# Kernel optimization log

Hardware: AMD Instinct MI355X
Metric: run time of the kernel (lower is better)

The kernel has to match this reference:

```python
import jax, jax.numpy as jnp
import numpy as np

B, N, C, H = 8, 1024, 1024, 16  # batch, seq, dim, heads
HID = 4 * C                     # mlp hidden (mlp_ratio=4.0)


def _ln(x, g, b, eps=1e-5):
    m = x.mean(-1, keepdims=True)
    v = ((x - m) ** 2).mean(-1, keepdims=True)
    return (x - m) / jnp.sqrt(v + eps) * g + b


def setup_inputs() -> dict:
    key = jax.random.key(0)
    ks = jax.random.split(key, 8)
    s = 0.02  # init scale
    f32 = jnp.float32
    return {
        "x": jax.random.normal(ks[0], (B, N, C), f32),
        "g1": jnp.ones((C,), f32), "b1": jnp.zeros((C,), f32),
        "Wq": jax.random.normal(ks[1], (C, C), f32) * s, "bq": jnp.zeros((C,), f32),
        "Wk": jax.random.normal(ks[2], (C, C), f32) * s, "bk": jnp.zeros((C,), f32),
        "Wv": jax.random.normal(ks[3], (C, C), f32) * s, "bv": jnp.zeros((C,), f32),
        "Wp": jax.random.normal(ks[4], (C, C), f32) * s, "bp": jnp.zeros((C,), f32),
        "g2": jnp.ones((C,), f32), "b2": jnp.zeros((C,), f32),
        "W1": jax.random.normal(ks[5], (C, HID), f32) * s, "c1": jnp.zeros((HID,), f32),
        "W2": jax.random.normal(ks[6], (HID, C), f32) * s, "c2": jnp.zeros((C,), f32),
    }


def reference(x, g1, b1, Wq, bq, Wk, bk, Wv, bv, Wp, bp, g2, b2, W1, c1, W2, c2):
    hd = C // H
    scale = hd ** -0.5
    # --- pre-norm self-attention ---
    h = _ln(x, g1, b1)
    # NOTE: faithful to source: direct reshape (B,N,C)->(B,H,N,hd), NOT the
    # standard reshape(B,N,H,hd).transpose -- the original code reshapes the
    # flat N*C block into H contiguous chunks of N*hd.
    q = (h @ Wq + bq).reshape(B, H, -1, hd)
    k = (h @ Wk + bk).reshape(B, H, -1, hd)
    v = (h @ Wv + bv).reshape(B, H, -1, hd)
    attn = jax.nn.softmax(jnp.einsum('bhnd,bhmd->bhnm', q, k) * scale, axis=-1)
    o = jnp.einsum('bhnm,bhmd->bhnd', attn, v)
    o = jnp.swapaxes(o, 1, 2).reshape(B, -1, C)  # (B,N,C)
    x = x + (o @ Wp + bp)
    # --- MLP block ---
    h2 = _ln(x, g2, b2)
    m = jax.nn.gelu(h2 @ W1 + c1, approximate=False) @ W2 + c2
    return x + m
```

## Files before the change

kernel.cpp:

```cpp
#include <hip/hip_runtime.h>
#include <hip/hip_bf16.h>
#include <math.h>

typedef __bf16 bf16_t;
typedef __bf16 bf16x4 __attribute__((ext_vector_type(4)));
typedef __bf16 bf16x8 __attribute__((ext_vector_type(8)));
typedef float  f32x4  __attribute__((ext_vector_type(4)));

typedef __attribute__((address_space(1))) const void GVoid;
typedef __attribute__((address_space(3))) void LVoid;

__device__ __forceinline__ void gld16(const void* g, void* l) {
    __builtin_amdgcn_global_load_lds((GVoid*)g, (LVoid*)l, 16, 0, 0);
}

__device__ __forceinline__ float gelu_exact(float v) {
    return 0.5f * v * (1.0f + erff(v * 0.7071067811865475f));
}

__device__ __forceinline__ f32x4 MF(bf16x8 a, bf16x8 b, f32x4 c) {
    return __builtin_amdgcn_mfma_f32_16x16x32_bf16(a, b, c, 0, 0, 0);
}

#define VMCNT(n) asm volatile("s_waitcnt vmcnt(" #n ")" ::: "memory")
#define FENCE()  asm volatile("" ::: "memory")

__global__ __launch_bounds__(256) void transpose_f32_bf16(
    const float* __restrict__ in, bf16_t* __restrict__ out,
    int R, int C, size_t inBatch, size_t outBatch)
{
    __shared__ bf16_t tile[64][65];
    const float* src = in  + (size_t)blockIdx.z * inBatch;
    bf16_t*      dst = out + (size_t)blockIdx.z * outBatch;
    const int r0 = blockIdx.y * 64, c0 = blockIdx.x * 64;
    const int t = threadIdx.x, tc = t & 63, tr = t >> 6;
#pragma unroll
    for (int i = 0; i < 16; ++i) {
        int r = tr + i * 4;
        tile[r][tc] = (bf16_t)src[(size_t)(r0 + r) * C + c0 + tc];
    }
    __syncthreads();
#pragma unroll
    for (int i = 0; i < 16; ++i) {
        int r = tr + i * 4;
        dst[(size_t)(c0 + r) * R + r0 + tc] = tile[tc][r];
    }
}

__global__ __launch_bounds__(256) void transpose_bf16(
    const bf16_t* __restrict__ in, bf16_t* __restrict__ out,
    int R, int C, size_t inBatch, size_t outBatch)
{
    __shared__ __align__(16) bf16_t tile[64][65];
    const bf16_t* src = in  + (size_t)blockIdx.z * inBatch;
    bf16_t*       dst = out + (size_t)blockIdx.z * outBatch;
    const int r0 = blockIdx.y * 64, c0 = blockIdx.x * 64;
    const int t = threadIdx.x, tc = t & 63, tr = t >> 6;
#pragma unroll
    for (int i = 0; i < 16; ++i) {
        int r = tr + i * 4;
        tile[r][tc] = src[(size_t)(r0 + r) * C + c0 + tc];
    }
    __syncthreads();
#pragma unroll
    for (int i = 0; i < 16; ++i) {
        int r = tr + i * 4;
        dst[(size_t)(c0 + r) * R + r0 + tc] = tile[tc][r];
    }
}

__global__ __launch_bounds__(256) void ln_kernel(
    const float* __restrict__ x, const float* __restrict__ g,
    const float* __restrict__ b, bf16_t* __restrict__ out)
{
    const int row = blockIdx.x, t = threadIdx.x;
    const float4 v4 = ((const float4*)(x + (size_t)row * 1024))[t];
    float v[4] = {v4.x, v4.y, v4.z, v4.w};
    float s = v[0] + v[1] + v[2] + v[3];
    float s2 = v[0]*v[0] + v[1]*v[1] + v[2]*v[2] + v[3]*v[3];
#pragma unroll
    for (int o = 1; o < 64; o <<= 1) { s += __shfl_xor(s, o); s2 += __shfl_xor(s2, o); }
    __shared__ float red[8];
    if ((t & 63) == 0) { red[t >> 6] = s; red[4 + (t >> 6)] = s2; }
    __syncthreads();
    s  = red[0] + red[1] + red[2] + red[3];
    s2 = red[4] + red[5] + red[6] + red[7];
    const float mean = s * (1.f / 1024.f);
    const float var  = fmaxf(s2 * (1.f / 1024.f) - mean * mean, 0.f);
    const float rstd = rsqrtf(var + 1e-5f);
    const float4 g4 = ((const float4*)g)[t];
    const float4 b4 = ((const float4*)b)[t];
    bf16x4 o;
    o[0] = (bf16_t)((v[0] - mean) * rstd * g4.x + b4.x);
    o[1] = (bf16_t)((v[1] - mean) * rstd * g4.y + b4.y);
    o[2] = (bf16_t)((v[2] - mean) * rstd * g4.z + b4.z);
    o[3] = (bf16_t)((v[3] - mean) * rstd * g4.w + b4.w);
    *(bf16x4*)(out + (size_t)row * 1024 + t * 4) = o;
}

template <int MODE>
__global__ __launch_bounds__(512, 2) void gemm256(
    const bf16_t* __restrict__ A, const bf16_t* __restrict__ Bt,
    const float* __restrict__ b0, const float* __restrict__ b1,
    const float* __restrict__ b2, const float* resid,
    bf16_t* __restrict__ ob0, bf16_t* __restrict__ ob1,
    bf16_t* __restrict__ ob2, float* of, int N, int K)
{
    __shared__ __align__(16) char lds[65536 + 32768];
    char* ldsB = lds + 65536;

    const int t = threadIdx.x;
    const int w = t >> 6, ln = t & 63;
    const int wm = w & 3, wn = w >> 2;
    const int l16 = ln & 15, quad = ln >> 4;
    const int m0 = blockIdx.x * 256, n0 = blockIdx.y * 128;

    const bf16_t* gA = A  + (size_t)m0 * K;
    const bf16_t* gB = Bt + (size_t)n0 * K;

    const int w1k  = w << 10;
    const int srow = t >> 3;
    const int scol = ((t & 7) ^ (srow & 7)) << 3;

    auto stageA = [&](int kt, int h) {
        char* dst = lds + (kt & 1) * 32768 + h * 16384 + w1k;
        const bf16_t* s0 = gA + (size_t)(h * 128 + srow) * K + (kt << 6) + scol;
        gld16(s0, dst);
        gld16(s0 + (size_t)64 * K, dst + 8192);
    };
    auto stageB = [&](int kt) {
        char* dst = ldsB + (kt & 1) * 16384 + w1k;
        const bf16_t* s0 = gB + (size_t)srow * K + (kt << 6) + scol;
        gld16(s0, dst);
        gld16(s0 + (size_t)64 * K, dst + 8192);
    };

    auto rdA = [&](int q, int i, int ks) -> bf16x8 {
        const int r = (i & 1) * 64 + wm * 16 + l16;
        const char* p = lds + q * 32768 + (i >> 1) * 16384 + r * 128
                        + ((ks * 64 + quad * 16) ^ ((r & 7) << 4));
        return *(const bf16x8*)p;
    };
    auto rdB = [&](int q, int j, int ks) -> bf16x8 {
        const int r = j * 32 + wn * 16 + l16;
        const char* p = ldsB + q * 16384 + r * 128
                        + ((ks * 64 + quad * 16) ^ ((r & 7) << 4));
        return *(const bf16x8*)p;
    };

    f32x4 acc[4][4];
#pragma unroll
    for (int i = 0; i < 4; ++i)
#pragma unroll
        for (int j = 0; j < 4; ++j) acc[i][j] = f32x4{0.f, 0.f, 0.f, 0.f};

    const int ktiles = K >> 6;

    stageA(0, 0); stageB(0); stageA(0, 1); stageA(1, 0); stageB(1);

    bf16x8 afr[2][2], bfr[4][2];

    for (int T = 0; T < ktiles; ++T) {
        const int q = T & 1;
        const bool notlast = (T + 1 < ktiles);

        if (notlast) VMCNT(6); else VMCNT(2);
        __builtin_amdgcn_s_barrier();
        FENCE(); __builtin_amdgcn_sched_barrier(0);
        if (notlast) stageA(T + 1, 1);
#pragma unroll
        for (int i = 0; i < 2; ++i)
#pragma unroll
            for (int ks = 0; ks < 2; ++ks) afr[i][ks] = rdA(q, i, ks);
#pragma unroll
        for (int j = 0; j < 4; ++j)
#pragma unroll
            for (int ks = 0; ks < 2; ++ks) bfr[j][ks] = rdB(q, j, ks);
        __builtin_amdgcn_s_setprio(1);
#pragma unroll
        for (int i = 0; i < 2; ++i)
#pragma unroll
            for (int j = 0; j < 4; ++j)
#pragma unroll
                for (int ks = 0; ks < 2; ++ks)
                    acc[i][j] = MF(afr[i][ks], bfr[j][ks], acc[i][j]);
        __builtin_amdgcn_s_setprio(0);
        __builtin_amdgcn_sched_barrier(0);

        if (notlast) VMCNT(6); else VMCNT(0);
        __builtin_amdgcn_s_barrier();
        FENCE(); __builtin_amdgcn_sched_barrier(0);
        if (T + 2 < ktiles) { stageA(T + 2, 0); stageB(T + 2); }
#pragma unroll
        for (int i = 0; i < 2; ++i)
#pragma unroll
            for (int ks = 0; ks < 2; ++ks) afr[i][ks] = rdA(q, 2 + i, ks);
        __builtin_amdgcn_s_setprio(1);
#pragma unroll
        for (int i = 0; i < 2; ++i)
#pragma unroll
            for (int j = 0; j < 4; ++j)
#pragma unroll
                for (int ks = 0; ks < 2; ++ks)
                    acc[2 + i][j] = MF(afr[i][ks], bfr[j][ks], acc[2 + i][j]);
        __builtin_amdgcn_s_setprio(0);
        __builtin_amdgcn_sched_barrier(0);
    }

#pragma unroll
    for (int i = 0; i < 4; ++i) {
        const int rowb = m0 + (i >> 1) * 128 + (i & 1) * 64 + wm * 16 + quad * 4;
#pragma unroll
        for (int j = 0; j < 4; ++j) {
            const int col = n0 + j * 32 + wn * 16 + l16;
            if constexpr (MODE == 0) {
                const int which = col >> 10;
                const float* bias = which == 0 ? b0 : (which == 1 ? b1 : b2);
                bf16_t* outp      = which == 0 ? ob0 : (which == 1 ? ob1 : ob2);
                const int cl = col & 1023;
                const float bc = bias[cl];
#pragma unroll
                for (int r = 0; r < 4; ++r)
                    outp[(size_t)(rowb + r) * 1024 + cl] = (bf16_t)(acc[i][j][r] + bc);
            } else if constexpr (MODE == 1) {
                const float bc = b0[col];
#pragma unroll
                for (int r = 0; r < 4; ++r) {
                    const size_t idx = (size_t)(rowb + r) * N + col;
                    of[idx] = acc[i][j][r] + bc + resid[idx];
                }
            } else if constexpr (MODE == 2) {
                const float bc = b0[col];
#pragma unroll
                for (int r = 0; r < 4; ++r)
                    ob0[(size_t)(rowb + r) * N + col] =
                        (bf16_t)gelu_exact(acc[i][j][r] + bc);
            } else {
#pragma unroll
                for (int r = 0; r < 4; ++r) {
                    const size_t idx = (size_t)(rowb + r) * N + col;
                    of[idx] += acc[i][j][r];
                }
            }
        }
    }
}

__global__ __launch_bounds__(256, 2) void attn_kernel(
    const bf16_t* __restrict__ Q, const bf16_t* __restrict__ K,
    const bf16_t* __restrict__ Vt, bf16_t* __restrict__ O)
{
    __shared__ __align__(16) bf16_t smem[32768];
    char* Vs = (char*)smem;
    char* Ks = (char*)smem + 16384;
    char* Ps = (char*)smem + 32768;

    const int t = threadIdx.x;
    const int wv = t >> 6, ln = t & 63;
    const int l16 = ln & 15, quad = ln >> 4;
    const int l7 = l16 & 7;
    const int lin = blockIdx.x + (blockIdx.y << 3);
    const int qt  = (lin >> 3) & 7;
    const int bh  = (lin & 7) * 16 + (lin >> 6);
    const size_t hb = (size_t)bh << 16;

    bf16x8 qf[2][2];
#pragma unroll
    for (int rt = 0; rt < 2; ++rt)
#pragma unroll
        for (int ks = 0; ks < 2; ++ks)
            qf[rt][ks] = *(const bf16x8*)(Q + hb +
                (size_t)(qt*128 + wv*32 + rt*16 + l16) * 64 + ks*32 + quad*8);

    float m_run[2] = {-INFINITY, -INFINITY};
    float l_run[2] = {0.f, 0.f};
    f32x4 acc_o[2][4];
#pragma unroll
    for (int rt = 0; rt < 2; ++rt)
#pragma unroll
        for (int dt = 0; dt < 4; ++dt) acc_o[rt][dt] = f32x4{0.f, 0.f, 0.f, 0.f};

    const int krow = t >> 3, kcol = (t & 7) << 3;
    const int vrow = t >> 4, vcol = (t & 15) << 3;
    const int kSwz = ((t & 7) ^ (krow & 7)) << 4;
    const int vSwz = ((t & 15) ^ (vrow & 7)) << 4;
    const float sc = 0.125f;

    bf16x8 kg[4], vg[4];
#pragma unroll
    for (int i = 0; i < 4; ++i) {
        kg[i] = *(const bf16x8*)(K  + hb + (size_t)(i*32 + krow)*64 + kcol);
        vg[i] = *(const bf16x8*)(Vt + hb + (size_t)(i*16 + vrow)*1024 + vcol);
    }

    for (int j = 0; j < 8; ++j) {
        __syncthreads();
#pragma unroll
        for (int i = 0; i < 4; ++i) {
            *(bf16x8*)(Ks + (i*32 + krow)*128 + kSwz) = kg[i];
            *(bf16x8*)(Vs + (i*16 + vrow)*256 + vSwz) = vg[i];
        }
        __syncthreads();
        if (j < 7) {
#pragma unroll
            for (int i = 0; i < 4; ++i) {
                kg[i] = *(const bf16x8*)(K  + hb + (size_t)((j+1)*128 + i*32 + krow)*64 + kcol);
                vg[i] = *(const bf16x8*)(Vt + hb + (size_t)(i*16 + vrow)*1024 + (j+1)*128 + vcol);
            }
        }

        f32x4 accs[8][2];
#pragma unroll
        for (int nt = 0; nt < 8; ++nt)
#pragma unroll
            for (int rt = 0; rt < 2; ++rt) accs[nt][rt] = f32x4{0.f, 0.f, 0.f, 0.f};
#pragma unroll
        for (int ks = 0; ks < 2; ++ks)
#pragma unroll
            for (int nt = 0; nt < 8; ++nt) {
                bf16x8 kf = *(const bf16x8*)(Ks + (nt*16 + l16)*128
                                             + (((ks*4 + quad) ^ l7) << 4));
#pragma unroll
                for (int rt = 0; rt < 2; ++rt)
                    accs[nt][rt] = __builtin_amdgcn_mfma_f32_16x16x32_bf16(
                        kf, qf[rt][ks], accs[nt][rt], 0, 0, 0);
            }

#pragma unroll
        for (int rt = 0; rt < 2; ++rt) {
            float mx = -INFINITY;
#pragma unroll
            for (int nt = 0; nt < 8; ++nt)
#pragma unroll
                for (int r = 0; r < 4; ++r) mx = fmaxf(mx, accs[nt][rt][r]);
            mx *= sc;
            mx = fmaxf(mx, __shfl_xor(mx, 16));
            mx = fmaxf(mx, __shfl_xor(mx, 32));
            if (!__all(mx <= m_run[rt] + 8.f)) {
                const float mnew  = fmaxf(m_run[rt], mx);
                const float alpha = __expf(m_run[rt] - mnew);
                m_run[rt] = mnew;
                l_run[rt] *= alpha;
#pragma unroll
                for (int r = 0; r < 4; ++r) {
                    const float af = __shfl(alpha, quad*4 + r, 16);
#pragma unroll
                    for (int dt = 0; dt < 4; ++dt) acc_o[rt][dt][r] *= af;
                }
            }
            const float mcur = m_run[rt];
            float rs = 0.f;
#pragma unroll
            for (int nt = 0; nt < 8; ++nt)
#pragma unroll
                for (int r = 0; r < 4; ++r) {
                    float p = __expf(accs[nt][rt][r] * sc - mcur);
                    accs[nt][rt][r] = p;
                    rs += p;
                }
            rs += __shfl_xor(rs, 16);
            rs += __shfl_xor(rs, 32);
            l_run[rt] += rs;
        }

#pragma unroll
        for (int rt = 0; rt < 2; ++rt) {
            const int mrow = wv*32 + rt*16 + l16;
#pragma unroll
            for (int nt = 0; nt < 8; ++nt) {
                bf16x4 pk;
#pragma unroll
                for (int r = 0; r < 4; ++r) pk[r] = (bf16_t)accs[nt][rt][r];
                const int pchunk = nt*2 + (quad >> 1);
                *(bf16x4*)(Ps + mrow*256 + ((pchunk ^ l7) << 4) + ((quad & 1) << 3)) = pk;
            }
        }
#pragma unroll
        for (int ks = 0; ks < 4; ++ks) {
            const int cSwz = ((ks*4 + quad) ^ l7) << 4;
            bf16x8 ap[2];
#pragma unroll
            for (int rt = 0; rt < 2; ++rt)
                ap[rt] = *(const bf16x8*)(Ps + (wv*32 + rt*16 + l16)*256 + cSwz);
#pragma unroll
            for (int dt = 0; dt < 4; ++dt) {
                bf16x8 bvv = *(const bf16x8*)(Vs + (dt*16 + l16)*256 + cSwz);
#pragma unroll
                for (int rt = 0; rt < 2; ++rt)
                    acc_o[rt][dt] = __builtin_amdgcn_mfma_f32_16x16x32_bf16(
                        ap[rt], bvv, acc_o[rt][dt], 0, 0, 0);
            }
        }
    }

    const int b = bh >> 4, h = bh & 15;
#pragma unroll
    for (int rt = 0; rt < 2; ++rt) {
#pragma unroll
        for (int r = 0; r < 4; ++r) {
            const float inv = 1.f / __shfl(l_run[rt], quad*4 + r, 16);
            const int m = qt*128 + wv*32 + rt*16 + quad*4 + r;
#pragma unroll
            for (int dt = 0; dt < 4; ++dt) {
                const int d = dt*16 + l16;
                O[((size_t)b*1024 + m)*1024 + h*64 + d] =
                    (bf16_t)(acc_o[rt][dt][r] * inv);
            }
        }
    }
}

extern "C" void kernel_launch(void* const* d_in, const int* in_sizes, int n_in,
                              void* d_out, int out_size, void* d_ws, size_t ws_size,
                              hipStream_t stream)
{
    (void)in_sizes; (void)n_in;
    const size_t MB = 1ull << 20;
    if (ws_size < 64 * MB) {
        hipMemsetAsync(d_out, 0, (size_t)out_size * sizeof(float), stream);
        return;
    }

    const float* x  = (const float*)d_in[0];
    const float* g1 = (const float*)d_in[1];
    const float* b1 = (const float*)d_in[2];
    const float* Wq = (const float*)d_in[3];
    const float* bq = (const float*)d_in[4];
    const float* Wk = (const float*)d_in[5];
    const float* bk = (const float*)d_in[6];
    const float* Wv = (const float*)d_in[7];
    const float* bv = (const float*)d_in[8];
    const float* Wp = (const float*)d_in[9];
    const float* bp = (const float*)d_in[10];
    const float* g2 = (const float*)d_in[11];
    const float* b2 = (const float*)d_in[12];
    const float* W1 = (const float*)d_in[13];
    const float* c1 = (const float*)d_in[14];
    const float* W2 = (const float*)d_in[15];
    const float* c2 = (const float*)d_in[16];

    char* ws = (char*)d_ws;
    bf16_t* Kb  = (bf16_t*)(ws);
    bf16_t* Vb  = (bf16_t*)(ws + 16 * MB);
    bf16_t* Cs  = (bf16_t*)(ws + 32 * MB);
    bf16_t* WqT = (bf16_t*)(ws + 48 * MB);
    bf16_t* WpT = (bf16_t*)(ws + 54 * MB);
    bf16_t* W1T = (bf16_t*)(ws + 56 * MB);
    bf16_t* W2T = (bf16_t*)(ws + 48 * MB);
    bf16_t* Qb  = (bf16_t*)d_out;
    bf16_t* Ob  = Vb;
    bf16_t* hid = Kb;
    bf16_t* h2  = Cs;
    float*  x2  = (float*)d_out;
    float*  outf = (float*)d_out;

    const dim3 blk(256);
    const dim3 blk5(512);

    transpose_f32_bf16<<<dim3(16, 16, 1), blk, 0, stream>>>(Wq, WqT,              1024, 1024, 0, 0);
    transpose_f32_bf16<<<dim3(16, 16, 1), blk, 0, stream>>>(Wk, WqT + 1024*1024,  1024, 1024, 0, 0);
    transpose_f32_bf16<<<dim3(16, 16, 1), blk, 0, stream>>>(Wv, WqT + 2*1024*1024, 1024, 1024, 0, 0);
    transpose_f32_bf16<<<dim3(16, 16, 1), blk, 0, stream>>>(Wp, WpT,              1024, 1024, 0, 0);
    transpose_f32_bf16<<<dim3(64, 16, 1), blk, 0, stream>>>(W1, W1T,              1024, 4096, 0, 0);

    ln_kernel<<<8192, blk, 0, stream>>>(x, g1, b1, Cs);

    gemm256<0><<<dim3(32, 24), blk5, 0, stream>>>(
        Cs, WqT, bq, bk, bv, nullptr, Qb, Kb, Vb, nullptr, 3072, 1024);

    transpose_bf16<<<dim3(1, 16, 128), blk, 0, stream>>>(Vb, Cs, 1024, 64, 65536, 65536);

    attn_kernel<<<dim3(8, 128), blk, 0, stream>>>(Qb, Kb, Cs, Ob);

    gemm256<1><<<dim3(32, 8), blk5, 0, stream>>>(
        Ob, WpT, bp, nullptr, nullptr, x, nullptr, nullptr, nullptr, x2, 1024, 1024);

    transpose_f32_bf16<<<dim3(16, 32, 2), blk, 0, stream>>>(
        W2, W2T, 2048, 1024, 2048*1024, 2048*1024);

    ln_kernel<<<8192, blk, 0, stream>>>(x2, g2, b2, h2);

    for (int c = 0; c < 2; ++c) {
        gemm256<2><<<dim3(32, 16), blk5, 0, stream>>>(
            h2, W1T + (size_t)c * 2048 * 1024, c1 + c * 2048,
            nullptr, nullptr, nullptr, hid, nullptr, nullptr, nullptr, 2048, 1024);
        if (c == 0)
            gemm256<1><<<dim3(32, 8), blk5, 0, stream>>>(
                hid, W2T, c2, nullptr, nullptr, outf,
                nullptr, nullptr, nullptr, outf, 1024, 2048);
        else
            gemm256<5><<<dim3(32, 8), blk5, 0, stream>>>(
                hid, W2T + (size_t)2048 * 1024, nullptr, nullptr, nullptr, nullptr,
                nullptr, nullptr, nullptr, outf, 1024, 2048);
    }
}
```

Before: 539.8 us.

## Add 256x256-tile 8-wave ping-pong GEMM for QKV and MLP-up projections

Introduces a new gemm8p kernel with a 256x256 output tile (each of 8 waves computes 128x64) and a finer-grained schedule. That schedule interleaves global-to-LDS staging of A/B halves with quadrant-wise MFMA blocks, separated by barriers and lgkmcnt waits. It is used for the QKV projection and the W1+GELU GEMMs to raise arithmetic intensity per LDS byte and halve B-tile global traffic. The old gemm256 remains for the residual-add GEMMs, with a trimmed signature. The cost is 128KB LDS per block and 128 accumulator registers per thread, which may limit occupancy. The many barriers could also expose latency.

```diff
diff --git a/kernel.cpp b/kernel.cpp
--- a/kernel.cpp
+++ b/kernel.cpp
@@ -24,6 +24,21 @@
 
 #define VMCNT(n) asm volatile("s_waitcnt vmcnt(" #n ")" ::: "memory")
 #define FENCE()  asm volatile("" ::: "memory")
+#define LG0()  do { asm volatile("s_waitcnt lgkmcnt(0)" ::: "memory"); \
+                    __builtin_amdgcn_sched_barrier(0); } while (0)
+#define BAR()  __builtin_amdgcn_s_barrier()
+
+#define MFQ(AARR, BARR, QR, QC)                                              \
+    do {                                                                     \
+        __builtin_amdgcn_s_setprio(1);                                       \
+        _Pragma("unroll") for (int rf = 0; rf < 4; ++rf)                     \
+        _Pragma("unroll") for (int cf = 0; cf < 2; ++cf)                     \
+        _Pragma("unroll") for (int ks = 0; ks < 2; ++ks)                     \
+            acc[(QR)*4 + rf][(QC)*2 + cf] =                                  \
+                MF(AARR[rf][ks], BARR[cf][ks], acc[(QR)*4 + rf][(QC)*2 + cf]); \
+        __builtin_amdgcn_s_setprio(0);                                       \
+        __builtin_amdgcn_sched_barrier(0);                                   \
+    } while (0)
 
 __global__ __launch_bounds__(256) void transpose_f32_bf16(
     const float* __restrict__ in, bf16_t* __restrict__ out,
@@ -99,21 +114,21 @@
 }
 
 template <int MODE>
-__global__ __launch_bounds__(512, 2) void gemm256(
+__global__ __launch_bounds__(512, 2) void gemm8p(
     const bf16_t* __restrict__ A, const bf16_t* __restrict__ Bt,
     const float* __restrict__ b0, const float* __restrict__ b1,
-    const float* __restrict__ b2, const float* resid,
+    const float* __restrict__ b2,
     bf16_t* __restrict__ ob0, bf16_t* __restrict__ ob1,
-    bf16_t* __restrict__ ob2, float* of, int N, int K)
+    bf16_t* __restrict__ ob2, int N, int K)
 {
-    __shared__ __align__(16) char lds[65536 + 32768];
+    __shared__ __align__(16) char lds[131072];
     char* ldsB = lds + 65536;
 
     const int t = threadIdx.x;
     const int w = t >> 6, ln = t & 63;
-    const int wm = w & 3, wn = w >> 2;
+    const int wm = w & 1, wn = w >> 1;
     const int l16 = ln & 15, quad = ln >> 4;
-    const int m0 = blockIdx.x * 256, n0 = blockIdx.y * 128;
+    const int m0 = blockIdx.x * 256, n0 = blockIdx.y * 256;
 
     const bf16_t* gA = A  + (size_t)m0 * K;
     const bf16_t* gB = Bt + (size_t)n0 * K;
@@ -128,91 +143,108 @@
         gld16(s0, dst);
         gld16(s0 + (size_t)64 * K, dst + 8192);
     };
-    auto stageB = [&](int kt) {
-        char* dst = ldsB + (kt & 1) * 16384 + w1k;
-        const bf16_t* s0 = gB + (size_t)srow * K + (kt << 6) + scol;
+    auto stageB = [&](int kt, int h) {
+        char* dst = ldsB + (kt & 1) * 32768 + h * 16384 + w1k;
+        const bf16_t* s0 = gB + (size_t)(h * 128 + srow) * K + (kt << 6) + scol;
         gld16(s0, dst);
         gld16(s0 + (size_t)64 * K, dst + 8192);
     };
 
-    auto rdA = [&](int q, int i, int ks) -> bf16x8 {
-        const int r = (i & 1) * 64 + wm * 16 + l16;
-        const char* p = lds + q * 32768 + (i >> 1) * 16384 + r * 128
-                        + ((ks * 64 + quad * 16) ^ ((r & 7) << 4));
-        return *(const bf16x8*)p;
-    };
-    auto rdB = [&](int q, int j, int ks) -> bf16x8 {
-        const int r = j * 32 + wn * 16 + l16;
-        const char* p = ldsB + q * 16384 + r * 128
-                        + ((ks * 64 + quad * 16) ^ ((r & 7) << 4));
-        return *(const bf16x8*)p;
-    };
-
-    f32x4 acc[4][4];
-#pragma unroll
-    for (int i = 0; i < 4; ++i)
+    auto rdAf = [&](int q, int h4, bf16x8 (&a)[4][2]) {
+#pragma unroll
+        for (int rf = 0; rf < 4; ++rf)
+#pragma unroll
+            for (int ks = 0; ks < 2; ++ks) {
+                const int lr = h4 * 64 + rf * 16 + l16;
+                a[rf][ks] = *(const bf16x8*)(lds + q * 32768 + wm * 16384
+                    + lr * 128 + ((ks * 64 + quad * 16) ^ ((lr & 7) << 4)));
+            }
+    };
+    auto rdBf = [&](int q, int qc, bf16x8 (&b)[2][2]) {
+#pragma unroll
+        for (int cf = 0; cf < 2; ++cf)
+#pragma unroll
+            for (int ks = 0; ks < 2; ++ks) {
+                const int lr = (wn & 1) * 64 + qc * 32 + cf * 16 + l16;
+                b[cf][ks] = *(const bf16x8*)(ldsB + q * 32768 + (wn >> 1) * 16384
+                    + lr * 128 + ((ks * 64 + quad * 16) ^ ((lr & 7) << 4)));
+            }
+    };
+
+    f32x4 acc[8][4];
+#pragma unroll
+    for (int i = 0; i < 8; ++i)
 #pragma unroll
         for (int j = 0; j < 4; ++j) acc[i][j] = f32x4{0.f, 0.f, 0.f, 0.f};
 
     const int ktiles = K >> 6;
 
-    stageA(0, 0); stageB(0); stageA(0, 1); stageA(1, 0); stageB(1);
-
-    bf16x8 afr[2][2], bfr[4][2];
-
-    for (int T = 0; T < ktiles; ++T) {
-        const int q = T & 1;
-        const bool notlast = (T + 1 < ktiles);
-
-        if (notlast) VMCNT(6); else VMCNT(2);
-        __builtin_amdgcn_s_barrier();
-        FENCE(); __builtin_amdgcn_sched_barrier(0);
-        if (notlast) stageA(T + 1, 1);
-#pragma unroll
-        for (int i = 0; i < 2; ++i)
-#pragma unroll
-            for (int ks = 0; ks < 2; ++ks) afr[i][ks] = rdA(q, i, ks);
-#pragma unroll
-        for (int j = 0; j < 4; ++j)
-#pragma unroll
-            for (int ks = 0; ks < 2; ++ks) bfr[j][ks] = rdB(q, j, ks);
-        __builtin_amdgcn_s_setprio(1);
-#pragma unroll
-        for (int i = 0; i < 2; ++i)
-#pragma unroll
-            for (int j = 0; j < 4; ++j)
-#pragma unroll
-                for (int ks = 0; ks < 2; ++ks)
-                    acc[i][j] = MF(afr[i][ks], bfr[j][ks], acc[i][j]);
-        __builtin_amdgcn_s_setprio(0);
-        __builtin_amdgcn_sched_barrier(0);
-
-        if (notlast) VMCNT(6); else VMCNT(0);
-        __builtin_amdgcn_s_barrier();
-        FENCE(); __builtin_amdgcn_sched_barrier(0);
-        if (T + 2 < ktiles) { stageA(T + 2, 0); stageB(T + 2); }
-#pragma unroll
-        for (int i = 0; i < 2; ++i)
-#pragma unroll
-            for (int ks = 0; ks < 2; ++ks) afr[i][ks] = rdA(q, 2 + i, ks);
-        __builtin_amdgcn_s_setprio(1);
-#pragma unroll
-        for (int i = 0; i < 2; ++i)
-#pragma unroll
-            for (int j = 0; j < 4; ++j)
-#pragma unroll
-                for (int ks = 0; ks < 2; ++ks)
-                    acc[2 + i][j] = MF(afr[i][ks], bfr[j][ks], acc[2 + i][j]);
-        __builtin_amdgcn_s_setprio(0);
-        __builtin_amdgcn_sched_barrier(0);
-    }
-
-#pragma unroll
-    for (int i = 0; i < 4; ++i) {
-        const int rowb = m0 + (i >> 1) * 128 + (i & 1) * 64 + wm * 16 + quad * 4;
+    stageA(0, 0); stageA(0, 1); stageB(0, 0); stageB(0, 1);
+    stageB(1, 0); stageA(1, 0);
+    VMCNT(4);
+    BAR();
+
+    bf16x8 aL[4][2], aH[4][2], bL[2][2], bH[2][2];
+
+    for (int it = 0; it < (ktiles >> 1); ++it) {
+        const int t0 = it * 2, t1 = t0 + 1;
+        const bool s2 = (t0 + 2 < ktiles), s3 = (t1 + 2 < ktiles);
+
+        stageA(t1, 1);
+        rdAf(0, 0, aL); rdBf(0, 0, bL);
+        BAR(); LG0();
+        MFQ(aL, bL, 0, 0);
+        BAR();
+
+        stageB(t1, 1);
+        rdBf(0, 1, bH);
+        BAR(); LG0();
+        MFQ(aL, bH, 0, 1);
+        BAR();
+
+        if (s2) stageB(t0 + 2, 0);
+        rdAf(0, 1, aH);
+        BAR(); LG0();
+        MFQ(aH, bH, 1, 1);
+        BAR();
+
+        if (s2) stageA(t0 + 2, 0);
+        BAR(); LG0();
+        MFQ(aH, bL, 1, 0);
+        if (s2) { VMCNT(4); } else { VMCNT(0); }
+        BAR();
+
+        if (s2) stageA(t0 + 2, 1);
+        rdAf(1, 0, aL); rdBf(1, 0, bL);
+        BAR(); LG0();
+        MFQ(aL, bL, 0, 0);
+        BAR();
+
+        if (s2) stageB(t0 + 2, 1);
+        rdBf(1, 1, bH);
+        BAR(); LG0();
+        MFQ(aL, bH, 0, 1);
+        BAR();
+
+        if (s3) stageB(t1 + 2, 0);
+        rdAf(1, 1, aH);
+        BAR(); LG0();
+        MFQ(aH, bH, 1, 1);
+        BAR();
+
+        if (s3) stageA(t1 + 2, 0);
+        BAR(); LG0();
+        MFQ(aH, bL, 1, 0);
+        if (s3) { VMCNT(4); } else { VMCNT(0); }
+        BAR();
+    }
+
+#pragma unroll
+    for (int i = 0; i < 8; ++i) {
+        const int rowb = m0 + wm * 128 + (i >> 2) * 64 + (i & 3) * 16 + quad * 4;
 #pragma unroll
         for (int j = 0; j < 4; ++j) {
-            const int col = n0 + j * 32 + wn * 16 + l16;
+            const int col = n0 + wn * 64 + j * 16 + l16;
             if constexpr (MODE == 0) {
                 const int which = col >> 10;
                 const float* bias = which == 0 ? b0 : (which == 1 ? b1 : b2);
@@ -222,19 +254,136 @@
 #pragma unroll
                 for (int r = 0; r < 4; ++r)
                     outp[(size_t)(rowb + r) * 1024 + cl] = (bf16_t)(acc[i][j][r] + bc);
-            } else if constexpr (MODE == 1) {
+            } else {
+                const float bc = b0[col];
+#pragma unroll
+                for (int r = 0; r < 4; ++r)
+                    ob0[(size_t)(rowb + r) * N + col] =
+                        (bf16_t)gelu_exact(acc[i][j][r] + bc);
+            }
+        }
+    }
+}
+
+template <int MODE>
+__global__ __launch_bounds__(512, 2) void gemm256(
+    const bf16_t* __restrict__ A, const bf16_t* __restrict__ Bt,
+    const float* __restrict__ b0, const float* resid, float* of, int N, int K)
+{
+    __shared__ __align__(16) char lds[65536 + 32768];
+    char* ldsB = lds + 65536;
+
+    const int t = threadIdx.x;
+    const int w = t >> 6, ln = t & 63;
+    const int wm = w & 3, wn = w >> 2;
+    const int l16 = ln & 15, quad = ln >> 4;
+    const int m0 = blockIdx.x * 256, n0 = blockIdx.y * 128;
+
+    const bf16_t* gA = A  + (size_t)m0 * K;
+    const bf16_t* gB = Bt + (size_t)n0 * K;
+
+    const int w1k  = w << 10;
+    const int srow = t >> 3;
+    const int scol = ((t & 7) ^ (srow & 7)) << 3;
+
+    auto stageA = [&](int kt, int h) {
+        char* dst = lds + (kt & 1) * 32768 + h * 16384 + w1k;
+        const bf16_t* s0 = gA + (size_t)(h * 128 + srow) * K + (kt << 6) + scol;
+        gld16(s0, dst);
+        gld16(s0 + (size_t)64 * K, dst + 8192);
+    };
+    auto stageB = [&](int kt) {
+        char* dst = ldsB + (kt & 1) * 16384 + w1k;
+        const bf16_t* s0 = gB + (size_t)srow * K + (kt << 6) + scol;
+        gld16(s0, dst);
+        gld16(s0 + (size_t)64 * K, dst + 8192);
+    };
+
+    auto rdA = [&](int q, int i, int ks) -> bf16x8 {
+        const int r = (i & 1) * 64 + wm * 16 + l16;
+        const char* p = lds + q * 32768 + (i >> 1) * 16384 + r * 128
+                        + ((ks * 64 + quad * 16) ^ ((r & 7) << 4));
+        return *(const bf16x8*)p;
+    };
+    auto rdB = [&](int q, int j, int ks) -> bf16x8 {
+        const int r = j * 32 + wn * 16 + l16;
+        const char* p = ldsB + q * 16384 + r * 128
+                        + ((ks * 64 + quad * 16) ^ ((r & 7) << 4));
+        return *(const bf16x8*)p;
+    };
+
+    f32x4 acc[4][4];
+#pragma unroll
+    for (int i = 0; i < 4; ++i)
+#pragma unroll
+        for (int j = 0; j < 4; ++j) acc[i][j] = f32x4{0.f, 0.f, 0.f, 0.f};
+
+    const int ktiles = K >> 6;
+
+    stageA(0, 0); stageB(0); stageA(0, 1); stageA(1, 0); stageB(1);
+
+    bf16x8 afr[2][2], bfr[4][2];
+
+    for (int T = 0; T < ktiles; ++T) {
+        const int q = T & 1;
+        const bool notlast = (T + 1 < ktiles);
+
+        if (notlast) VMCNT(6); else VMCNT(2);
+        BAR();
+        FENCE(); __builtin_amdgcn_sched_barrier(0);
+        if (notlast) stageA(T + 1, 1);
+#pragma unroll
+        for (int i = 0; i < 2; ++i)
+#pragma unroll
+            for (int ks = 0; ks < 2; ++ks) afr[i][ks] = rdA(q, i, ks);
+#pragma unroll
+        for (int j = 0; j < 4; ++j)
+#pragma unroll
+            for (int ks = 0; ks < 2; ++ks) bfr[j][ks] = rdB(q, j, ks);
+        __builtin_amdgcn_s_setprio(1);
+#pragma unroll
+        for (int i = 0; i < 2; ++i)
+#pragma unroll
+            for (int j = 0; j < 4; ++j)
+#pragma unroll
+                for (int ks = 0; ks < 2; ++ks)
+                    acc[i][j] = MF(afr[i][ks], bfr[j][ks], acc[i][j]);
+        __builtin_amdgcn_s_setprio(0);
+        __builtin_amdgcn_sched_barrier(0);
+
+        if (notlast) VMCNT(6); else VMCNT(0);
+        BAR();
+        FENCE(); __builtin_amdgcn_sched_barrier(0);
+        if (T + 2 < ktiles) { stageA(T + 2, 0); stageB(T + 2); }
+#pragma unroll
+        for (int i = 0; i < 2; ++i)
+#pragma unroll
+            for (int ks = 0; ks < 2; ++ks) afr[i][ks] = rdA(q, 2 + i, ks);
+        __builtin_amdgcn_s_setprio(1);
+#pragma unroll
+        for (int i = 0; i < 2; ++i)
+#pragma unroll
+            for (int j = 0; j < 4; ++j)
+#pragma unroll
+                for (int ks = 0; ks < 2; ++ks)
+                    acc[2 + i][j] = MF(afr[i][ks], bfr[j][ks], acc[2 + i][j]);
+        __builtin_amdgcn_s_setprio(0);
+        __builtin_amdgcn_sched_barrier(0);
+    }
+
+#pragma unroll
+    for (int i = 0; i < 4; ++i) {
+        const int rowb = m0 + (i >> 1) * 128 + (i & 1) * 64 + wm * 16 + quad * 4;
+#pragma unroll
+        for (int j = 0; j < 4; ++j) {
+            const int col = n0 + j * 32 + wn * 16 + l16;
+            if constexpr (MODE == 1) {
                 const float bc = b0[col];
 #pragma unroll
                 for (int r = 0; r < 4; ++r) {
                     const size_t idx = (size_t)(rowb + r) * N + col;
                     of[idx] = acc[i][j][r] + bc + resid[idx];
                 }
-            } else if constexpr (MODE == 2) {
-                const float bc = b0[col];
-#pragma unroll
-                for (int r = 0; r < 4; ++r)
-                    ob0[(size_t)(rowb + r) * N + col] =
-                        (bf16_t)gelu_exact(acc[i][j][r] + bc);
             } else {
 #pragma unroll
                 for (int r = 0; r < 4; ++r) {
@@ -465,15 +614,15 @@
 
     ln_kernel<<<8192, blk, 0, stream>>>(x, g1, b1, Cs);
 
-    gemm256<0><<<dim3(32, 24), blk5, 0, stream>>>(
-        Cs, WqT, bq, bk, bv, nullptr, Qb, Kb, Vb, nullptr, 3072, 1024);
+    gemm8p<0><<<dim3(32, 12), blk5, 0, stream>>>(
+        Cs, WqT, bq, bk, bv, Qb, Kb, Vb, 3072, 1024);
 
     transpose_bf16<<<dim3(1, 16, 128), blk, 0, stream>>>(Vb, Cs, 1024, 64, 65536, 65536);
 
     attn_kernel<<<dim3(8, 128), blk, 0, stream>>>(Qb, Kb, Cs, Ob);
 
     gemm256<1><<<dim3(32, 8), blk5, 0, stream>>>(
-        Ob, WpT, bp, nullptr, nullptr, x, nullptr, nullptr, nullptr, x2, 1024, 1024);
+        Ob, WpT, bp, x, x2, 1024, 1024);
 
     transpose_f32_bf16<<<dim3(16, 32, 2), blk, 0, stream>>>(
         W2, W2T, 2048, 1024, 2048*1024, 2048*1024);
@@ -481,16 +630,14 @@
     ln_kernel<<<8192, blk, 0, stream>>>(x2, g2, b2, h2);
 
     for (int c = 0; c < 2; ++c) {
-        gemm256<2><<<dim3(32, 16), blk5, 0, stream>>>(
+        gemm8p<2><<<dim3(32, 8), blk5, 0, stream>>>(
             h2, W1T + (size_t)c * 2048 * 1024, c1 + c * 2048,
-            nullptr, nullptr, nullptr, hid, nullptr, nullptr, nullptr, 2048, 1024);
+            nullptr, nullptr, hid, nullptr, nullptr, 2048, 1024);
         if (c == 0)
             gemm256<1><<<dim3(32, 8), blk5, 0, stream>>>(
-                hid, W2T, c2, nullptr, nullptr, outf,
-                nullptr, nullptr, nullptr, outf, 1024, 2048);
+                hid, W2T, c2, outf, outf, 1024, 2048);
         else
             gemm256<5><<<dim3(32, 8), blk5, 0, stream>>>(
-                hid, W2T + (size_t)2048 * 1024, nullptr, nullptr, nullptr, nullptr,
-                nullptr, nullptr, nullptr, outf, 1024, 2048);
-    }
-}
+                hid, W2T + (size_t)2048 * 1024, nullptr, nullptr, outf, 1024, 2048);
+    }
+}
```

After: 614.5 us. 1.14x slower.

## Swizzle GEMM workgroups across XCDs and merge weight transpose launches

Applied to the files above, without the earlier changes.

Remaps each GEMM workgroup's linear index so that the workgroups placed on the same XCD handle neighbouring output tiles, improving L2 reuse of the A and B panels. Also folds the four square weight transposes into one launch using blockIdx.z to pick the source, cutting launch overhead. The remap hardcodes 32 row tiles per column and assumes the workgroup count is divisible by 8.

```diff
diff --git a/kernel.cpp b/kernel.cpp
--- a/kernel.cpp
+++ b/kernel.cpp
@@ -44,6 +44,30 @@
     for (int i = 0; i < 16; ++i) {
         int r = tr + i * 4;
         dst[(size_t)(c0 + r) * R + r0 + tc] = tile[tc][r];
+    }
+}
+
+__global__ __launch_bounds__(256) void transpose4_w(
+    const float* __restrict__ w0, const float* __restrict__ w1,
+    const float* __restrict__ w2, const float* __restrict__ w3,
+    bf16_t* __restrict__ out0, bf16_t* __restrict__ out3)
+{
+    __shared__ bf16_t tile[64][65];
+    const int z = blockIdx.z;
+    const float* src = z == 0 ? w0 : (z == 1 ? w1 : (z == 2 ? w2 : w3));
+    bf16_t* dst = z == 3 ? out3 : out0 + (size_t)z * 1024 * 1024;
+    const int r0 = blockIdx.y * 64, c0 = blockIdx.x * 64;
+    const int t = threadIdx.x, tc = t & 63, tr = t >> 6;
+#pragma unroll
+    for (int i = 0; i < 16; ++i) {
+        int r = tr + i * 4;
+        tile[r][tc] = (bf16_t)src[(size_t)(r0 + r) * 1024 + c0 + tc];
+    }
+    __syncthreads();
+#pragma unroll
+    for (int i = 0; i < 16; ++i) {
+        int r = tr + i * 4;
+        dst[(size_t)(c0 + r) * 1024 + r0 + tc] = tile[tc][r];
     }
 }
 
@@ -113,7 +137,11 @@
     const int w = t >> 6, ln = t & 63;
     const int wm = w & 3, wn = w >> 2;
     const int l16 = ln & 15, quad = ln >> 4;
-    const int m0 = blockIdx.x * 256, n0 = blockIdx.y * 128;
+
+    const int nwg = gridDim.x * gridDim.y;
+    const int lin = blockIdx.x + blockIdx.y * gridDim.x;
+    const int nl  = (lin & 7) * (nwg >> 3) + (lin >> 3);
+    const int m0 = (nl & 31) * 256, n0 = (nl >> 5) * 128;
 
     const bf16_t* gA = A  + (size_t)m0 * K;
     const bf16_t* gB = Bt + (size_t)n0 * K;
@@ -457,11 +485,8 @@
     const dim3 blk(256);
     const dim3 blk5(512);
 
-    transpose_f32_bf16<<<dim3(16, 16, 1), blk, 0, stream>>>(Wq, WqT,              1024, 1024, 0, 0);
-    transpose_f32_bf16<<<dim3(16, 16, 1), blk, 0, stream>>>(Wk, WqT + 1024*1024,  1024, 1024, 0, 0);
-    transpose_f32_bf16<<<dim3(16, 16, 1), blk, 0, stream>>>(Wv, WqT + 2*1024*1024, 1024, 1024, 0, 0);
-    transpose_f32_bf16<<<dim3(16, 16, 1), blk, 0, stream>>>(Wp, WpT,              1024, 1024, 0, 0);
-    transpose_f32_bf16<<<dim3(64, 16, 1), blk, 0, stream>>>(W1, W1T,              1024, 4096, 0, 0);
+    transpose4_w<<<dim3(16, 16, 4), blk, 0, stream>>>(Wq, Wk, Wv, Wp, WqT, WpT);
+    transpose_f32_bf16<<<dim3(64, 16, 1), blk, 0, stream>>>(W1, W1T, 1024, 4096, 0, 0);
 
     ln_kernel<<<8192, blk, 0, stream>>>(x, g1, b1, Cs);
 
```

Result: slower. 570.1 us (+5.6%).
